# Performance work log

Measured on AMD Instinct MI355X. Metric: run time of the kernel, lower is better.

The kernel has to match this reference:

```python
import jax, jax.numpy as jnp
import numpy as np

N, C, H, W = 8, 256, 128, 128
HD = 256          # hidden_depth
FC, FS, CS = 8, 2, 8  # heads_count, fold_size, center_size
EPS_GN = 1e-5


def setup_inputs() -> dict:
    key = jax.random.key(0)
    ks = jax.random.split(key, 8)
    d = {
        'x': jax.random.normal(ks[0], (N, C, H, W), jnp.float32),
        'proj_w': jax.random.normal(ks[1], (2 * HD, C), jnp.float32) * 0.02,
        'proj_b': jnp.zeros((2 * HD,), jnp.float32),
        'merge_w': jax.random.normal(ks[2], (C, HD), jnp.float32) * 0.02,
        'merge_b': jnp.zeros((C,), jnp.float32),
        'alpha': jnp.ones((1,), jnp.float32),
        'beta': jnp.zeros((1,), jnp.float32),
        'g0_w': jnp.ones((C,), jnp.float32),
        'g0_b': jnp.zeros((C,), jnp.float32),
        'mlp_w0': jax.random.normal(ks[3], (2 * C, 2 * C), jnp.float32) * 0.02,
        'mlp_b0': jnp.zeros((2 * C,), jnp.float32),
        'mlp_w1': jax.random.normal(ks[4], (2 * C, C), jnp.float32) * 0.02,
        'mlp_b1': jnp.zeros((C,), jnp.float32),
        'g1_w': jnp.ones((C,), jnp.float32),
        'g1_b': jnp.zeros((C,), jnp.float32),
        'layer_scale': jnp.full((C,), 1e-5, jnp.float32),
    }
    return d


def _group_norm1(x, w, b):
    # GroupNorm(1, C): normalize over (C,H,W) per sample, per-channel affine
    mu = x.mean(axis=(1, 2, 3), keepdims=True)
    var = ((x - mu) ** 2).mean(axis=(1, 2, 3), keepdims=True)
    xn = (x - mu) * jax.lax.rsqrt(var + EPS_GN)
    return xn * w[None, :, None, None] + b[None, :, None, None]


def _l2norm(v):
    return v / jnp.maximum(jnp.linalg.norm(v, axis=-1, keepdims=True), 1e-12)


def _local_cluster(x, proj_w, proj_b, merge_w, merge_b, alpha, beta):
    n = x.shape[0]
    # 1x1 conv proj: C -> 2*HD
    y = jnp.einsum('nchw,oc->nohw', x, proj_w) + proj_b[None, :, None, None]
    c = y.shape[1] // FC              # per-head channels (2*HD/FC)
    h, w = H // FS, W // FS
    # 'n (fc c) (fh h) (fw w) -> (n fc fh fw) c h w'
    y = y.reshape(n, FC, c, FS, h, FS, w).transpose(0, 1, 3, 5, 2, 4, 6)
    y = y.reshape(n * FC * FS * FS, c, h, w)
    m = y.shape[0]
    # adaptive avg pool to CSxCS (h,w divisible by CS -> uniform pooling)
    center = y.reshape(m, c, CS, h // CS, CS, w // CS).mean(axis=(3, 5))
    L, s = h * w, CS * CS
    yf = y.reshape(m, c, L).transpose(0, 2, 1)       # [m, L, c]
    cf = center.reshape(m, c, s).transpose(0, 2, 1)  # [m, s, c]
    cv = c // 2
    x_point, x_value = yf[..., :cv], yf[..., cv:]
    c_point, c_value = cf[..., :cv], cf[..., cv:]
    sim = jnp.einsum('mlc,msc->mls', _l2norm(x_point), _l2norm(c_point))
    sim = jax.nn.sigmoid(alpha * sim + beta)         # [m, L, s]
    vals = sim.max(axis=2)                           # [m, L]
    idx = sim.argmax(axis=2) + s * jnp.arange(m)[:, None]
    vals = vals.reshape(-1)
    idx = idx.reshape(-1)
    xv = x_value.reshape(-1, cv)
    cvv = c_value.reshape(-1, cv)
    xv_aug = jnp.concatenate([xv, jnp.ones((xv.shape[0], 1), xv.dtype)], axis=1)
    cv_aug = jnp.concatenate([cvv, jnp.ones((cvv.shape[0], 1), cvv.dtype)], axis=1)
    # scatter-add weighted points into centers
    nc = cv_aug.at[idx].add(vals[:, None] * xv_aug)
    nc = nc[:, :-1] / nc[:, -1:]
    # gather back
    nx = vals[:, None] * nc[idx]                     # [m*L, cv]
    # '(n fc fh fw h w) c -> n (fc c) (fh h) (fw w)'
    nx = nx.reshape(n, FC, FS, FS, h, w, cv).transpose(0, 1, 6, 2, 4, 3, 5)
    nx = nx.reshape(n, FC * cv, H, W)                # [n, HD, H, W]
    return jnp.einsum('nchw,oc->nohw', nx, merge_w) + merge_b[None, :, None, None]


def reference(x, proj_w, proj_b, merge_w, merge_b, alpha, beta, g0_w, g0_b,
              mlp_w0, mlp_b0, mlp_w1, mlp_b1, g1_w, g1_b, layer_scale):
    new_x = _local_cluster(x, proj_w, proj_b, merge_w, merge_b, alpha, beta)
    new_x = _group_norm1(new_x, g0_w, g0_b)
    t = jnp.concatenate([x, new_x], axis=1)          # [n, 2C, H, W]
    t = t.transpose(0, 2, 3, 1)                      # NHWC
    t = jax.nn.gelu(t @ mlp_w0 + mlp_b0, approximate=False)
    t = t @ mlp_w1 + mlp_b1
    t = t.transpose(0, 3, 1, 2)                      # NCHW
    t = _group_norm1(t, g1_w, g1_b)
    t = t * layer_scale[None, :, None, None]
    return t + x
```

## Files before the change

### kernel.cpp

```cpp
#include <hip/hip_runtime.h>
#include <math.h>

#define PIX   16384
#define NB    8
#define CIN   256

typedef __attribute__((ext_vector_type(8))) short    short8;
typedef __attribute__((ext_vector_type(4))) float    f32x4;
typedef __attribute__((ext_vector_type(4))) unsigned short us4;
typedef __attribute__((ext_vector_type(8))) unsigned short us8;

__device__ __forceinline__ float bf2f(unsigned short h) {
  return __uint_as_float(((unsigned int)h) << 16);
}
__device__ __forceinline__ unsigned short f2bf(float f) {
  unsigned int u = __float_as_uint(f);
  return (unsigned short)((u + 0x7FFFu + ((u >> 16) & 1u)) >> 16);
}
__device__ __forceinline__ float gelu_f(float v) {
  return 0.5f * v * (1.f + erff(v * 0.70710678118654752f));
}

__device__ __forceinline__ float rowmax16(float v) {
  v = fmaxf(v, __uint_as_float(__builtin_amdgcn_update_dpp(
        __float_as_uint(v), __float_as_uint(v), 0x121, 0xF, 0xF, false)));
  v = fmaxf(v, __uint_as_float(__builtin_amdgcn_update_dpp(
        __float_as_uint(v), __float_as_uint(v), 0x122, 0xF, 0xF, false)));
  v = fmaxf(v, __uint_as_float(__builtin_amdgcn_update_dpp(
        __float_as_uint(v), __float_as_uint(v), 0x124, 0xF, 0xF, false)));
  v = fmaxf(v, __uint_as_float(__builtin_amdgcn_update_dpp(
        __float_as_uint(v), __float_as_uint(v), 0x128, 0xF, 0xF, false)));
  return v;
}

__global__ void zero_kernel(float* p, int n) {
  int i = blockIdx.x * blockDim.x + threadIdx.x;
  if (i < n) p[i] = 0.f;
}

__global__ void prep_weights(const float* __restrict__ pw_f, const float* __restrict__ mw_f,
                             const float* __restrict__ w0, const float* __restrict__ w1,
                             unsigned short* __restrict__ pw, unsigned short* __restrict__ mw,
                             unsigned short* __restrict__ w0t, unsigned short* __restrict__ w1t) {
  const int S1 = 512 * 256, S2 = 256 * 256, S3 = 512 * 512, S4 = 256 * 512;
  int i = blockIdx.x * 256 + threadIdx.x;
  if (i < S1) { pw[i] = f2bf(pw_f[i]); return; }
  i -= S1;
  if (i < S2) { mw[i] = f2bf(mw_f[i]); return; }
  i -= S2;
  if (i < S3) { int o = i >> 9, k = i & 511; w0t[i] = f2bf(w0[k * 512 + o]); return; }
  i -= S3;
  if (i < S4) { int o = i >> 9, k = i & 511; w1t[i] = f2bf(w1[k * 256 + o]); }
}

__global__ __launch_bounds__(256) void x_to_nhwc(const float* __restrict__ x,
                                                 unsigned short* __restrict__ xT) {
  __shared__ float tile[64][65];
  const int t = threadIdx.x;
  const int p0 = blockIdx.x * 64, c0 = blockIdx.y * 64, n = blockIdx.z;
#pragma unroll
  for (int i = 0; i < 4; i++) {
    const int c = i * 16 + (t >> 4);
    const float4 v = *(const float4*)(x + ((size_t)(n * 256 + c0 + c) << 14) + p0 + (t & 15) * 4);
    tile[c][(t & 15) * 4]     = v.x;
    tile[c][(t & 15) * 4 + 1] = v.y;
    tile[c][(t & 15) * 4 + 2] = v.z;
    tile[c][(t & 15) * 4 + 3] = v.w;
  }
  __syncthreads();
#pragma unroll
  for (int i = 0; i < 4; i++) {
    const int pp = i * 16 + (t >> 4);
    const int cl = (t & 15) * 4;
    us4 o;
    o.x = f2bf(tile[cl][pp]); o.y = f2bf(tile[cl + 1][pp]);
    o.z = f2bf(tile[cl + 2][pp]); o.w = f2bf(tile[cl + 3][pp]);
    *(us4*)&xT[(((size_t)n << 14) + p0 + pp) * 256 + c0 + cl] = o;
  }
}

template<bool CONCAT, bool GELU, bool STATS>
__global__ __launch_bounds__(256, 2) void mfma_gemm(
    const unsigned short* __restrict__ A, const float* __restrict__ bias,
    const unsigned short* __restrict__ B1, const unsigned short* __restrict__ B2,
    unsigned short* __restrict__ Y, int M, int K, int K1,
    int astride, int bstride, float* __restrict__ sums) {
  __shared__ unsigned short As[8192];
  __shared__ unsigned short Bs[8192];
  __shared__ float r1[4], r2[4];
  const int t = threadIdx.x;
  const int lane = t & 63, w = t >> 6;
  const int quad = lane >> 4, l16 = lane & 15;
  const int p0 = blockIdx.x * 128, m0 = blockIdx.y * 128;
  const int n = blockIdx.z;
  const int wm = w & 1, wn = w >> 1;
  const int K2 = K - K1;

  A += (size_t)n * astride;

  f32x4 acc[4][4];
#pragma unroll
  for (int im = 0; im < 4; im++)
#pragma unroll
    for (int in = 0; in < 4; in++) acc[im][in] = (f32x4)0.f;

  for (int k0 = 0; k0 < K; k0 += 64) {
    __syncthreads();
#pragma unroll
    for (int i = 0; i < 4; i++) {
      const int c = (w << 2) | i;
      const int tm = c >> 1, kk = c & 1;
      const int krow = k0 + kk * 32 + quad * 8;
      const unsigned short* ga = A + (size_t)(m0 + tm * 16 + l16) * K + krow;
      __builtin_amdgcn_global_load_lds((const __attribute__((address_space(1))) void*)ga,
          (__attribute__((address_space(3))) void*)&As[c * 512], 16, 0, 0);
      const int prow = p0 + tm * 16 + l16;
      const unsigned short* gb;
      if (!CONCAT || krow < K1)
        gb = B1 + ((((size_t)n << 14) + prow) * (size_t)K1) + krow;
      else
        gb = B2 + ((((size_t)n << 14) + prow) * (size_t)K2) + (krow - K1);
      __builtin_amdgcn_global_load_lds((const __attribute__((address_space(1))) void*)gb,
          (__attribute__((address_space(3))) void*)&Bs[c * 512], 16, 0, 0);
    }
    __syncthreads();
#pragma unroll
    for (int kk = 0; kk < 2; kk++) {
      short8 af[4], bfr[4];
#pragma unroll
      for (int im = 0; im < 4; im++)
        af[im] = *(const short8*)&As[(((wm * 4 + im) * 2 + kk) * 64 + lane) * 8];
#pragma unroll
      for (int in = 0; in < 4; in++)
        bfr[in] = *(const short8*)&Bs[(((wn * 4 + in) * 2 + kk) * 64 + lane) * 8];
#pragma unroll
      for (int im = 0; im < 4; im++)
#pragma unroll
        for (int in = 0; in < 4; in++)
          acc[im][in] = __builtin_amdgcn_mfma_f32_16x16x32_bf16(af[im], bfr[in], acc[im][in], 0, 0, 0);
    }
  }

  const size_t nb = ((size_t)n << 14);
  float s = 0.f, s2 = 0.f;
#pragma unroll
  for (int im = 0; im < 4; im++) {
    const int om = m0 + (wm * 4 + im) * 16 + quad * 4;
    const f32x4 bv = *(const f32x4*)(bias + (size_t)n * bstride + om);
#pragma unroll
    for (int in = 0; in < 4; in++) {
      const int p = p0 + (wn * 4 + in) * 16 + l16;
      float v0 = acc[im][in].x + bv.x;
      float v1 = acc[im][in].y + bv.y;
      float v2 = acc[im][in].z + bv.z;
      float v3 = acc[im][in].w + bv.w;
      if (GELU) { v0 = gelu_f(v0); v1 = gelu_f(v1); v2 = gelu_f(v2); v3 = gelu_f(v3); }
      if (STATS) {
        s += (v0 + v1) + (v2 + v3);
        s2 = fmaf(v0, v0, s2); s2 = fmaf(v1, v1, s2);
        s2 = fmaf(v2, v2, s2); s2 = fmaf(v3, v3, s2);
      }
      us4 o4;
      o4.x = f2bf(v0); o4.y = f2bf(v1); o4.z = f2bf(v2); o4.w = f2bf(v3);
      *(us4*)&Y[(nb + p) * M + om] = o4;
    }
  }
  if (STATS) {
#pragma unroll
    for (int off = 32; off > 0; off >>= 1) {
      s += __shfl_down(s, off);
      s2 += __shfl_down(s2, off);
    }
    if (lane == 0) { r1[w] = s; r2[w] = s2; }
    __syncthreads();
    if (t == 0) {
      atomicAdd(&sums[2 * n],     (r1[0] + r1[1]) + (r1[2] + r1[3]));
      atomicAdd(&sums[2 * n + 1], (r2[0] + r2[1]) + (r2[2] + r2[3]));
    }
  }
}


__global__ __launch_bounds__(256) void centers_kernel(
    const unsigned short* __restrict__ y, unsigned short* __restrict__ cpnh_g,
    float* __restrict__ cval_g) {
  const int m = blockIdx.y, slice = blockIdx.x;
  const int n = m >> 5, f = (m >> 2) & 7, s1 = (m >> 1) & 1, s2 = m & 1;
  const int t = threadIdx.x;
  __shared__ float cs[16][68];

  const size_t nbase = ((size_t)n << 14);
  const int prow0 = s1 * 64, pcol0 = s2 * 64, ch0 = f * 64;

  {
    const int bl = t >> 4;
    const int b = slice * 16 + bl;
    const int tid = t & 15, cg = tid & 7, ph = tid >> 3;
    const int pr0 = prow0 + (b >> 3) * 8 + ph * 4;
    const int pc0 = pcol0 + (b & 7) * 8;
    const unsigned short* yb = y + (nbase + (size_t)pr0 * 128 + pc0) * 512 + ch0 + cg * 8;
    float a8[8] = {0.f, 0.f, 0.f, 0.f, 0.f, 0.f, 0.f, 0.f};
#pragma unroll
    for (int r = 0; r < 4; r++) {
      us8 buf[8];
#pragma unroll
      for (int cc = 0; cc < 8; cc++)
        buf[cc] = *(const us8*)(yb + ((size_t)r * 128 + cc) * 512);
#pragma unroll
      for (int cc = 0; cc < 8; cc++)
#pragma unroll
        for (int j = 0; j < 8; j++) a8[j] += bf2f(buf[cc][j]);
    }
#pragma unroll
    for (int j = 0; j < 8; j++) a8[j] += __shfl_xor(a8[j], 8);
    if (ph == 0) {
      f32x4 o0, o1;
      o0.x = a8[0] * (1.f / 64.f); o0.y = a8[1] * (1.f / 64.f);
      o0.z = a8[2] * (1.f / 64.f); o0.w = a8[3] * (1.f / 64.f);
      o1.x = a8[4] * (1.f / 64.f); o1.y = a8[5] * (1.f / 64.f);
      o1.z = a8[6] * (1.f / 64.f); o1.w = a8[7] * (1.f / 64.f);
      *(f32x4*)&cs[bl][cg * 8]     = o0;
      *(f32x4*)&cs[bl][cg * 8 + 4] = o1;
    }
  }
  __syncthreads();

  if (t < 128) {
    const int bl = t >> 3, jg = t & 7;
    const int bg = slice * 16 + bl;
    if (jg < 8) {
      f32x4 ov;
      ov.x = cs[bl][32 + jg * 4]; ov.y = cs[bl][32 + jg * 4 + 1];
      ov.z = cs[bl][32 + jg * 4 + 2]; ov.w = cs[bl][32 + jg * 4 + 3];
      *(f32x4*)&cval_g[((size_t)(m * 64 + bg) << 5) + jg * 4] = ov;
    }
    float s = 0.f;
#pragma unroll
    for (int cc = 0; cc < 32; cc++) { const float v = cs[bl][cc]; s = fmaf(v, v, s); }
    const float inv = 1.f / fmaxf(sqrtf(s), 1e-12f);
    us4 o;
    o.x = f2bf(cs[bl][jg * 4] * inv);     o.y = f2bf(cs[bl][jg * 4 + 1] * inv);
    o.z = f2bf(cs[bl][jg * 4 + 2] * inv); o.w = f2bf(cs[bl][jg * 4 + 3] * inv);
    *(us4*)&cpnh_g[((size_t)(m * 64 + bg) << 5) + jg * 4] = o;
  }
}

__global__ __launch_bounds__(256, 8) void assign_kernel(
    const unsigned short* __restrict__ y, const unsigned short* __restrict__ cpnh_g,
    const float* __restrict__ alpha_p, const float* __restrict__ beta_p,
    float* __restrict__ svals_g, unsigned char* __restrict__ sbest_g,
    float* __restrict__ accp_v, float* __restrict__ accp_c) {
  const int m = blockIdx.y, slice = blockIdx.x;
  const int n = m >> 5, f = (m >> 2) & 7, s1 = (m >> 1) & 1, s2 = m & 1;
  const int t = threadIdx.x;
  const int wave = t >> 6, lane = t & 63;
  const int quad = lane >> 4, l16 = lane & 15;
  const float alpha = alpha_p[0], beta = beta_p[0];

  __shared__ float accv[64][34];

  for (int i = t; i < 64 * 34; i += 256) ((float*)accv)[i] = 0.f;

  const size_t nbase = ((size_t)n << 14);
  const int prow0 = s1 * 64, pcol0 = s2 * 64, ch0 = f * 64;

  const short8 cb0 = *(const short8*)&cpnh_g[((size_t)(m * 64 +  0 + l16) << 5) + quad * 8];
  const short8 cb1 = *(const short8*)&cpnh_g[((size_t)(m * 64 + 16 + l16) << 5) + quad * 8];
  const short8 cb2 = *(const short8*)&cpnh_g[((size_t)(m * 64 + 32 + l16) << 5) + quad * 8];
  const short8 cb3 = *(const short8*)&cpnh_g[((size_t)(m * 64 + 48 + l16) << 5) + quad * 8];
  const int sl4 = (((l16 >> 2) << 4) | (l16 & 3)) << 2;
  const int sh = quad << 4;
  __syncthreads();

  auto loadpt = [&](int tile, short8& a, short8& v) {
    const int pidx = slice * 512 + wave * 128 + tile * 16;
    const int pix = (prow0 + (pidx >> 6)) * 128 + pcol0 + (pidx & 63) + l16;
    const unsigned short* yp = y + (nbase + pix) * 512 + ch0 + quad * 8;
    a = *(const short8*)yp;
    v = *(const short8*)(yp + 32);
  };

  auto compute_tile = [&](int tile, short8 apt, short8 avl) {
    const int pidx = slice * 512 + wave * 128 + tile * 16;

    float nrm = 0.f;
#pragma unroll
    for (int j = 0; j < 8; j++) {
      const float fv = bf2f((unsigned short)apt[j]);
      nrm = fmaf(fv, fv, nrm);
    }
    nrm += __shfl_xor(nrm, 16);
    nrm += __shfl_xor(nrm, 32);
    const float inva = 1.f / fmaxf(sqrtf(nrm), 1e-12f);

    const f32x4 d0 = __builtin_amdgcn_mfma_f32_16x16x32_bf16(apt, cb0, (f32x4)0.f, 0, 0, 0);
    const f32x4 d1 = __builtin_amdgcn_mfma_f32_16x16x32_bf16(apt, cb1, (f32x4)0.f, 0, 0, 0);
    const f32x4 d2 = __builtin_amdgcn_mfma_f32_16x16x32_bf16(apt, cb2, (f32x4)0.f, 0, 0, 0);
    const f32x4 d3 = __builtin_amdgcn_mfma_f32_16x16x32_bf16(apt, cb3, (f32x4)0.f, 0, 0, 0);

    float bv[4]; int bi[4];
#pragma unroll
    for (int r = 0; r < 4; r++) {
      float v = fmaxf(fmaxf(d0[r], d1[r]), fmaxf(d2[r], d3[r]));
      v = rowmax16(v);
      bv[r] = v;
      const unsigned long long m0 = __ballot(d0[r] == v);
      const unsigned long long m1 = __ballot(d1[r] == v);
      const unsigned long long m2 = __ballot(d2[r] == v);
      const unsigned long long m3 = __ballot(d3[r] == v);
      const unsigned f0 = (unsigned)(m0 >> sh) & 0xFFFFu;
      const unsigned f1 = (unsigned)(m1 >> sh) & 0xFFFFu;
      const unsigned f2 = (unsigned)(m2 >> sh) & 0xFFFFu;
      const unsigned f3 = (unsigned)(m3 >> sh) & 0xFFFFu;
      int ii = 48 + __ffs(f3) - 1;
      if (f2) ii = 32 + __ffs(f2) - 1;
      if (f1) ii = 16 + __ffs(f1) - 1;
      if (f0) ii = __ffs(f0) - 1;
      bi[r] = ii;
    }

    const float rv01 = (l16 & 1) ? bv[1] : bv[0];
    const float rv23 = (l16 & 1) ? bv[3] : bv[2];
    const float rowv = (l16 & 2) ? rv23 : rv01;
    const int   ri01 = (l16 & 1) ? bi[1] : bi[0];
    const int   ri23 = (l16 & 1) ? bi[3] : bi[2];
    const int   rowi = (l16 & 2) ? ri23 : ri01;
    const unsigned pk = (__float_as_uint(rowv) & ~63u) | (unsigned)rowi;
    const unsigned got = (unsigned)__builtin_amdgcn_ds_bpermute(sl4, (int)pk);
    const int   idx = (int)(got & 63u);
    const float dot = __uint_as_float(got & ~63u);

    const float val = 1.f / (1.f + __expf(-fmaf(alpha, dot * inva, beta)));
    if (quad == 0) {
      svals_g[(size_t)m * 4096 + pidx + l16] = val;
      sbest_g[(size_t)m * 4096 + pidx + l16] = (unsigned char)idx;
    }
#pragma unroll
    for (int j = 0; j < 8; j++)
      atomicAdd(&accv[idx][quad * 8 + j], val * bf2f((unsigned short)avl[j]));
    if (quad == 0) atomicAdd(&accv[idx][32], val);
  };

  {
    short8 a0, v0, a1 = {}, v1 = {};
    loadpt(0, a0, v0);
#pragma unroll 1
    for (int tp = 0; tp < 8; tp++) {
      if (tp < 7) loadpt(tp + 1, a1, v1);
      compute_tile(tp, a0, v0);
      a0 = a1; v0 = v1;
    }
  }
  __syncthreads();

  const size_t pb = ((size_t)(m * 8 + slice)) * 64;
  for (int i = t; i < 2048; i += 256) {
    const int b = i >> 5, q = i & 31;
    accp_v[(pb + b) * 32 + q] = accv[b][q];
  }
  if (t < 64) accp_c[pb + t] = accv[t][32];
}

__global__ __launch_bounds__(256) void gather_kernel(
    const float* __restrict__ accp_v, const float* __restrict__ accp_c,
    const float* __restrict__ cval_g, const float* __restrict__ svals_g,
    const unsigned char* __restrict__ sbest_g, unsigned short* __restrict__ nx) {
  const int m = blockIdx.y, slice = blockIdx.x;
  const int n = m >> 5, f = (m >> 2) & 7, s1 = (m >> 1) & 1, s2 = m & 1;
  const int t = threadIdx.x;
  __shared__ float cm[64][34];

  const size_t nbase = ((size_t)n << 14);
  const int prow0 = s1 * 64, pcol0 = s2 * 64;

  for (int i = t; i < 2048; i += 256) {
    const int b = i >> 5, q = i & 31;
    float s = cval_g[((size_t)(m * 64 + b) << 5) + q];
    float c = 1.f;
#pragma unroll
    for (int s8 = 0; s8 < 8; s8++) {
      const size_t pb = ((size_t)(m * 8 + s8)) * 64 + b;
      s += accp_v[pb * 32 + q];
      c += accp_c[pb];
    }
    cm[b][q] = s / c;
  }
  __syncthreads();

#pragma unroll
  for (int pass = 0; pass < 2; pass++) {
    const int l = slice * 512 + pass * 256 + t;
    const int p = (prow0 + (l >> 6)) * 128 + pcol0 + (l & 63);
    const float v = svals_g[(size_t)m * 4096 + l];
    const int b = sbest_g[(size_t)m * 4096 + l];
    unsigned short* nr = nx + (nbase + p) * 256 + f * 32;
#pragma unroll
    for (int q8 = 0; q8 < 4; q8++) {
      const float2 a0 = *(const float2*)&cm[b][q8 * 8];
      const float2 a1 = *(const float2*)&cm[b][q8 * 8 + 2];
      const float2 a2 = *(const float2*)&cm[b][q8 * 8 + 4];
      const float2 a3 = *(const float2*)&cm[b][q8 * 8 + 6];
      us8 o;
      o[0] = f2bf(v * a0.x); o[1] = f2bf(v * a0.y);
      o[2] = f2bf(v * a1.x); o[3] = f2bf(v * a1.y);
      o[4] = f2bf(v * a2.x); o[5] = f2bf(v * a2.y);
      o[6] = f2bf(v * a3.x); o[7] = f2bf(v * a3.y);
      *(us8*)&nr[q8 * 8] = o;
    }
  }
}

__global__ void gn_finalize0(const float* __restrict__ sums, const float* __restrict__ g0w,
                             const float* __restrict__ g0b, float* __restrict__ scl,
                             float* __restrict__ bia) {
  const int n = blockIdx.x, c = threadIdx.x;
  const float cntinv = 1.f / (float)(CIN * PIX);
  const float mu = sums[2 * n] * cntinv;
  const float var = sums[2 * n + 1] * cntinv - mu * mu;
  const float rs = rsqrtf(var + 1e-5f);
  const float a = rs * g0w[c];
  scl[n * 256 + c] = a;
  bia[n * 256 + c] = g0b[c] - mu * a;
}

__global__ void w0_scale(const unsigned short* __restrict__ w0t,
                         const float* __restrict__ scl, unsigned short* __restrict__ w0s) {
  const int n = blockIdx.y;
  const int i = blockIdx.x * 256 + threadIdx.x;
  const int k = i & 511;
  unsigned short v = w0t[i];
  if (k >= 256) v = f2bf(bf2f(v) * scl[n * 256 + k - 256]);
  w0s[(size_t)n * 262144 + i] = v;
}

__global__ void b0_eff(const unsigned short* __restrict__ w0t, const float* __restrict__ b0,
                       const float* __restrict__ bia, float* __restrict__ b0e) {
  const int n = blockIdx.y;
  const int o = blockIdx.x * 256 + threadIdx.x;
  float s = b0[o];
  const unsigned short* wr = w0t + (size_t)o * 512 + 256;
  const float* br = bia + n * 256;
#pragma unroll 4
  for (int k = 0; k < 256; k++) s = fmaf(bf2f(wr[k]), br[k], s);
  b0e[n * 512 + o] = s;
}

__global__ __launch_bounds__(256) void final_transpose(
    const unsigned short* __restrict__ u, const float* __restrict__ x,
    const float* __restrict__ sums, const float* __restrict__ g1w,
    const float* __restrict__ g1b, const float* __restrict__ lsc,
    float* __restrict__ out) {
  __shared__ float tile[64][68];
  const int t = threadIdx.x;
  const int p0 = blockIdx.x * 64, c0 = blockIdx.y * 64, n = blockIdx.z;
  {
    const int pl = t >> 2, g = t & 3;
    const unsigned short* up = u + ((((size_t)n << 14) + p0 + pl) << 8) + c0 + g * 16;
    const us8 v0 = *(const us8*)up;
    const us8 v1 = *(const us8*)(up + 8);
#pragma unroll
    for (int j = 0; j < 8; j++) {
      tile[pl][g * 16 + j] = bf2f(v0[j]);
      tile[pl][g * 16 + 8 + j] = bf2f(v1[j]);
    }
  }
  __syncthreads();
  {
    const int cl = t >> 2, g = t & 3;
    const int c = c0 + cl;
    const float cntinv = 1.f / (float)(CIN * PIX);
    const float mu = sums[2 * n] * cntinv;
    const float var = sums[2 * n + 1] * cntinv - mu * mu;
    const float rs = rsqrtf(var + 1e-5f);
    const float gw = rs * g1w[c] * lsc[c];
    const float gb = (g1b[c] - mu * rs * g1w[c]) * lsc[c];
    const size_t rowb = ((size_t)(n * 256 + c) << 14) + p0 + g * 16;
#pragma unroll
    for (int q = 0; q < 4; q++) {
      const float4 xv = *(const float4*)(x + rowb + q * 4);
      float4 o;
      o.x = fmaf(tile[g * 16 + q * 4][cl], gw, gb) + xv.x;
      o.y = fmaf(tile[g * 16 + q * 4 + 1][cl], gw, gb) + xv.y;
      o.z = fmaf(tile[g * 16 + q * 4 + 2][cl], gw, gb) + xv.z;
      o.w = fmaf(tile[g * 16 + q * 4 + 3][cl], gw, gb) + xv.w;
      *(float4*)(out + rowb + q * 4) = o;
    }
  }
}

extern "C" void kernel_launch(void* const* d_in, const int* in_sizes, int n_in,
                              void* d_out, int out_size, void* d_ws, size_t ws_size,
                              hipStream_t stream) {
  const float* x       = (const float*)d_in[0];
  const float* proj_w  = (const float*)d_in[1];
  const float* proj_b  = (const float*)d_in[2];
  const float* merge_w = (const float*)d_in[3];
  const float* merge_b = (const float*)d_in[4];
  const float* alpha   = (const float*)d_in[5];
  const float* beta    = (const float*)d_in[6];
  const float* g0w     = (const float*)d_in[7];
  const float* g0b     = (const float*)d_in[8];
  const float* w0      = (const float*)d_in[9];
  const float* b0      = (const float*)d_in[10];
  const float* w1      = (const float*)d_in[11];
  const float* b1      = (const float*)d_in[12];
  const float* g1w     = (const float*)d_in[13];
  const float* g1b     = (const float*)d_in[14];
  const float* lsc     = (const float*)d_in[15];
  float* out = (float*)d_out;

  unsigned short* wsu = (unsigned short*)d_ws;
  unsigned short* xT  = wsu;
  unsigned short* y   = xT + (size_t)33554432;
  unsigned short* nx  = y + (size_t)67108864;
  unsigned short* pw  = nx + (size_t)33554432;
  unsigned short* mw  = pw + 131072;
  unsigned short* w0t = mw + 65536;
  unsigned short* w1t = w0t + 262144;
  unsigned short* w0s = w1t + 131072;
  float* sums = (float*)(w0s + (size_t)2097152);
  float* scl0 = sums + 32;
  float* bia0 = scl0 + 2048;
  float* b0e  = bia0 + 2048;
  unsigned short* newx = (unsigned short*)d_out;

  float* svals_g = (float*)((char*)d_out + 67108864);
  float* cval_g  = svals_g + 1048576;
  float* accp_v  = cval_g + 524288;
  float* accp_c  = accp_v + 4194304;
  unsigned short* cpnh_g = (unsigned short*)(accp_c + 131072);
  unsigned char*  sbest_g = (unsigned char*)(cpnh_g + 524288);

  zero_kernel<<<1, 64, 0, stream>>>(sums, 32);
  prep_weights<<<2304, 256, 0, stream>>>(proj_w, merge_w, w0, w1, pw, mw, w0t, w1t);
  x_to_nhwc<<<dim3(256, 4, NB), 256, 0, stream>>>(x, xT);

  mfma_gemm<false, false, false><<<dim3(128, 4, NB), 256, 0, stream>>>(
      pw, proj_b, xT, nullptr, y, 512, 256, 256, 0, 0, nullptr);

  centers_kernel<<<dim3(4, 256), 256, 0, stream>>>(y, cpnh_g, cval_g);
  assign_kernel<<<dim3(8, 256), 256, 0, stream>>>(
      y, cpnh_g, alpha, beta, svals_g, sbest_g, accp_v, accp_c);
  gather_kernel<<<dim3(8, 256), 256, 0, stream>>>(
      accp_v, accp_c, cval_g, svals_g, sbest_g, nx);

  mfma_gemm<false, false, true><<<dim3(128, 2, NB), 256, 0, stream>>>(
      mw, merge_b, nx, nullptr, newx, 256, 256, 256, 0, 0, sums);

  gn_finalize0<<<NB, 256, 0, stream>>>(sums, g0w, g0b, scl0, bia0);
  w0_scale<<<dim3(1024, NB), 256, 0, stream>>>(w0t, scl0, w0s);
  b0_eff<<<dim3(2, NB), 256, 0, stream>>>(w0t, b0, bia0, b0e);

  mfma_gemm<true, true, false><<<dim3(128, 4, NB), 256, 0, stream>>>(
      w0s, b0e, xT, newx, y, 512, 512, 256, 262144, 512, nullptr);

  mfma_gemm<false, false, true><<<dim3(128, 2, NB), 256, 0, stream>>>(
      w1t, b1, y, nullptr, nx, 256, 512, 512, 0, 0, sums + 16);

  final_transpose<<<dim3(256, 4, NB), 256, 0, stream>>>(
      nx, x, sums + 16, g1w, g1b, lsc, out);
}
```

Measured before the change: 1.007 ms.

## Load GEMM fragments directly from global memory; hoist assign loads; compile-time K

The MFMA GEMM no longer stages A and B tiles through LDS with global_load_lds and barriers. Each wave now reads its bf16 fragments straight from global memory into registers, and K is a template constant so the loop fully unrolls. The assign kernel issues all eight tile loads up front before computing, and its occupancy hint drops from 8 to 4 blocks per SM to allow more registers. The aim is to remove LDS round-trips and barrier stalls, at the cost of redundant global or cache traffic and higher register pressure.

```diff
diff --git a/kernel.cpp b/kernel.cpp
--- a/kernel.cpp
+++ b/kernel.cpp
@@ -79,14 +79,12 @@
   }
 }
 
-template<bool CONCAT, bool GELU, bool STATS>
-__global__ __launch_bounds__(256, 2) void mfma_gemm(
+template<int KI, int K1I, bool CONCAT, bool GELU, bool STATS>
+__global__ __launch_bounds__(256, 2) void mfma_gemm_v2(
     const unsigned short* __restrict__ A, const float* __restrict__ bias,
     const unsigned short* __restrict__ B1, const unsigned short* __restrict__ B2,
-    unsigned short* __restrict__ Y, int M, int K, int K1,
+    unsigned short* __restrict__ Y, int M,
     int astride, int bstride, float* __restrict__ sums) {
-  __shared__ unsigned short As[8192];
-  __shared__ unsigned short Bs[8192];
   __shared__ float r1[4], r2[4];
   const int t = threadIdx.x;
   const int lane = t & 63, w = t >> 6;
@@ -94,9 +92,15 @@
   const int p0 = blockIdx.x * 128, m0 = blockIdx.y * 128;
   const int n = blockIdx.z;
   const int wm = w & 1, wn = w >> 1;
-  const int K2 = K - K1;
+  constexpr int K2I = (KI - K1I) > 0 ? (KI - K1I) : 1;
 
   A += (size_t)n * astride;
+  const size_t nb = ((size_t)n << 14);
+
+  const unsigned short* abase  = A + (size_t)(m0 + wm * 64 + l16) * KI + quad * 8;
+  const unsigned short* b1base = B1 + (nb + p0 + wn * 64 + l16) * (size_t)K1I + quad * 8;
+  const unsigned short* b2base = CONCAT
+      ? B2 + (nb + p0 + wn * 64 + l16) * (size_t)K2I + quad * 8 : B1;
 
   f32x4 acc[4][4];
 #pragma unroll
@@ -104,44 +108,26 @@
 #pragma unroll
     for (int in = 0; in < 4; in++) acc[im][in] = (f32x4)0.f;
 
-  for (int k0 = 0; k0 < K; k0 += 64) {
-    __syncthreads();
-#pragma unroll
-    for (int i = 0; i < 4; i++) {
-      const int c = (w << 2) | i;
-      const int tm = c >> 1, kk = c & 1;
-      const int krow = k0 + kk * 32 + quad * 8;
-      const unsigned short* ga = A + (size_t)(m0 + tm * 16 + l16) * K + krow;
-      __builtin_amdgcn_global_load_lds((const __attribute__((address_space(1))) void*)ga,
-          (__attribute__((address_space(3))) void*)&As[c * 512], 16, 0, 0);
-      const int prow = p0 + tm * 16 + l16;
-      const unsigned short* gb;
-      if (!CONCAT || krow < K1)
-        gb = B1 + ((((size_t)n << 14) + prow) * (size_t)K1) + krow;
+#pragma unroll
+  for (int ks = 0; ks < KI / 32; ks++) {
+    short8 af[4], bfr[4];
+#pragma unroll
+    for (int im = 0; im < 4; im++)
+      af[im] = *(const short8*)(abase + (size_t)im * 16 * KI + ks * 32);
+#pragma unroll
+    for (int in = 0; in < 4; in++) {
+      if (!CONCAT || (ks * 32) < K1I)
+        bfr[in] = *(const short8*)(b1base + (size_t)in * 16 * K1I + ks * 32);
       else
-        gb = B2 + ((((size_t)n << 14) + prow) * (size_t)K2) + (krow - K1);
-      __builtin_amdgcn_global_load_lds((const __attribute__((address_space(1))) void*)gb,
-          (__attribute__((address_space(3))) void*)&Bs[c * 512], 16, 0, 0);
-    }
-    __syncthreads();
-#pragma unroll
-    for (int kk = 0; kk < 2; kk++) {
-      short8 af[4], bfr[4];
-#pragma unroll
-      for (int im = 0; im < 4; im++)
-        af[im] = *(const short8*)&As[(((wm * 4 + im) * 2 + kk) * 64 + lane) * 8];
+        bfr[in] = *(const short8*)(b2base + (size_t)in * 16 * K2I + (ks * 32 - K1I));
+    }
+#pragma unroll
+    for (int im = 0; im < 4; im++)
 #pragma unroll
       for (int in = 0; in < 4; in++)
-        bfr[in] = *(const short8*)&Bs[(((wn * 4 + in) * 2 + kk) * 64 + lane) * 8];
-#pragma unroll
-      for (int im = 0; im < 4; im++)
-#pragma unroll
-        for (int in = 0; in < 4; in++)
-          acc[im][in] = __builtin_amdgcn_mfma_f32_16x16x32_bf16(af[im], bfr[in], acc[im][in], 0, 0, 0);
-    }
-  }
-
-  const size_t nb = ((size_t)n << 14);
+        acc[im][in] = __builtin_amdgcn_mfma_f32_16x16x32_bf16(af[im], bfr[in], acc[im][in], 0, 0, 0);
+  }
+
   float s = 0.f, s2 = 0.f;
 #pragma unroll
   for (int im = 0; im < 4; im++) {
@@ -245,7 +231,7 @@
   }
 }
 
-__global__ __launch_bounds__(256, 8) void assign_kernel(
+__global__ __launch_bounds__(256, 4) void assign_kernel(
     const unsigned short* __restrict__ y, const unsigned short* __restrict__ cpnh_g,
     const float* __restrict__ alpha_p, const float* __restrict__ beta_p,
     float* __restrict__ svals_g, unsigned char* __restrict__ sbest_g,
@@ -342,14 +328,13 @@
   };
 
   {
-    short8 a0, v0, a1 = {}, v1 = {};
-    loadpt(0, a0, v0);
-#pragma unroll 1
-    for (int tp = 0; tp < 8; tp++) {
-      if (tp < 7) loadpt(tp + 1, a1, v1);
-      compute_tile(tp, a0, v0);
-      a0 = a1; v0 = v1;
-    }
+    short8 a0, v0, a1, v1, a2, v2, a3, v3, a4, v4, a5, v5, a6, v6, a7, v7;
+    loadpt(0, a0, v0); loadpt(1, a1, v1); loadpt(2, a2, v2); loadpt(3, a3, v3);
+    loadpt(4, a4, v4); loadpt(5, a5, v5); loadpt(6, a6, v6); loadpt(7, a7, v7);
+    compute_tile(0, a0, v0); compute_tile(1, a1, v1);
+    compute_tile(2, a2, v2); compute_tile(3, a3, v3);
+    compute_tile(4, a4, v4); compute_tile(5, a5, v5);
+    compute_tile(6, a6, v6); compute_tile(7, a7, v7);
   }
   __syncthreads();
 
@@ -535,8 +520,8 @@
   prep_weights<<<2304, 256, 0, stream>>>(proj_w, merge_w, w0, w1, pw, mw, w0t, w1t);
   x_to_nhwc<<<dim3(256, 4, NB), 256, 0, stream>>>(x, xT);
 
-  mfma_gemm<false, false, false><<<dim3(128, 4, NB), 256, 0, stream>>>(
-      pw, proj_b, xT, nullptr, y, 512, 256, 256, 0, 0, nullptr);
+  mfma_gemm_v2<256, 256, false, false, false><<<dim3(128, 4, NB), 256, 0, stream>>>(
+      pw, proj_b, xT, nullptr, y, 512, 0, 0, nullptr);
 
   centers_kernel<<<dim3(4, 256), 256, 0, stream>>>(y, cpnh_g, cval_g);
   assign_kernel<<<dim3(8, 256), 256, 0, stream>>>(
@@ -544,18 +529,18 @@
   gather_kernel<<<dim3(8, 256), 256, 0, stream>>>(
       accp_v, accp_c, cval_g, svals_g, sbest_g, nx);
 
-  mfma_gemm<false, false, true><<<dim3(128, 2, NB), 256, 0, stream>>>(
-      mw, merge_b, nx, nullptr, newx, 256, 256, 256, 0, 0, sums);
+  mfma_gemm_v2<256, 256, false, false, true><<<dim3(128, 2, NB), 256, 0, stream>>>(
+      mw, merge_b, nx, nullptr, newx, 256, 0, 0, sums);
 
   gn_finalize0<<<NB, 256, 0, stream>>>(sums, g0w, g0b, scl0, bia0);
   w0_scale<<<dim3(1024, NB), 256, 0, stream>>>(w0t, scl0, w0s);
   b0_eff<<<dim3(2, NB), 256, 0, stream>>>(w0t, b0, bia0, b0e);
 
-  mfma_gemm<true, true, false><<<dim3(128, 4, NB), 256, 0, stream>>>(
-      w0s, b0e, xT, newx, y, 512, 512, 256, 262144, 512, nullptr);
-
-  mfma_gemm<false, false, true><<<dim3(128, 2, NB), 256, 0, stream>>>(
-      w1t, b1, y, nullptr, nx, 256, 512, 512, 0, 0, sums + 16);
+  mfma_gemm_v2<512, 256, true, true, false><<<dim3(128, 4, NB), 256, 0, stream>>>(
+      w0s, b0e, xT, newx, y, 512, 262144, 512, nullptr);
+
+  mfma_gemm_v2<512, 512, false, false, true><<<dim3(128, 2, NB), 256, 0, stream>>>(
+      w1t, b1, y, nullptr, nx, 256, 0, 0, sums + 16);
 
   final_transpose<<<dim3(256, 4, NB), 256, 0, stream>>>(
       nx, x, sums + 16, g1w, g1b, lsc, out);
```

Measured after the change: 1.197 ms. +18.9%, slower.

## Replace ballot argmax with DPP integer reductions, preload all tiles, retune launch bounds

Applied to the files above, without the earlier changes.

The per-row argmax in assign_kernel now maps floats to monotone unsigned keys, reduces the max with DPP, and finds the first matching index with a DPP integer min, replacing four ballots plus ffs logic. All eight point tiles are loaded up front instead of software-pipelined one tile ahead, which exposes more memory parallelism at the cost of registers. To allow for that, assign_kernel's launch bounds drop from 8 to 4 waves per SIMD, while mfma_gemm's rise from 2 to 4, which may force register spilling in the GEMM.

```diff
diff --git a/kernel.cpp b/kernel.cpp
--- a/kernel.cpp
+++ b/kernel.cpp
@@ -21,15 +21,25 @@
   return 0.5f * v * (1.f + erff(v * 0.70710678118654752f));
 }
 
-__device__ __forceinline__ float rowmax16(float v) {
-  v = fmaxf(v, __uint_as_float(__builtin_amdgcn_update_dpp(
-        __float_as_uint(v), __float_as_uint(v), 0x121, 0xF, 0xF, false)));
-  v = fmaxf(v, __uint_as_float(__builtin_amdgcn_update_dpp(
-        __float_as_uint(v), __float_as_uint(v), 0x122, 0xF, 0xF, false)));
-  v = fmaxf(v, __uint_as_float(__builtin_amdgcn_update_dpp(
-        __float_as_uint(v), __float_as_uint(v), 0x124, 0xF, 0xF, false)));
-  v = fmaxf(v, __uint_as_float(__builtin_amdgcn_update_dpp(
-        __float_as_uint(v), __float_as_uint(v), 0x128, 0xF, 0xF, false)));
+__device__ __forceinline__ unsigned fmono(float f) {
+  const unsigned u = __float_as_uint(f);
+  return (u & 0x80000000u) ? ~u : (u | 0x80000000u);
+}
+
+__device__ __forceinline__ unsigned umax16(unsigned v) {
+  unsigned t;
+  t = (unsigned)__builtin_amdgcn_update_dpp((int)v, (int)v, 0x121, 0xF, 0xF, false); v = v > t ? v : t;
+  t = (unsigned)__builtin_amdgcn_update_dpp((int)v, (int)v, 0x122, 0xF, 0xF, false); v = v > t ? v : t;
+  t = (unsigned)__builtin_amdgcn_update_dpp((int)v, (int)v, 0x124, 0xF, 0xF, false); v = v > t ? v : t;
+  t = (unsigned)__builtin_amdgcn_update_dpp((int)v, (int)v, 0x128, 0xF, 0xF, false); v = v > t ? v : t;
+  return v;
+}
+__device__ __forceinline__ int imin16(int v) {
+  int t;
+  t = __builtin_amdgcn_update_dpp(v, v, 0x121, 0xF, 0xF, false); v = v < t ? v : t;
+  t = __builtin_amdgcn_update_dpp(v, v, 0x122, 0xF, 0xF, false); v = v < t ? v : t;
+  t = __builtin_amdgcn_update_dpp(v, v, 0x124, 0xF, 0xF, false); v = v < t ? v : t;
+  t = __builtin_amdgcn_update_dpp(v, v, 0x128, 0xF, 0xF, false); v = v < t ? v : t;
   return v;
 }
 
@@ -80,7 +90,7 @@
 }
 
 template<bool CONCAT, bool GELU, bool STATS>
-__global__ __launch_bounds__(256, 2) void mfma_gemm(
+__global__ __launch_bounds__(256, 4) void mfma_gemm(
     const unsigned short* __restrict__ A, const float* __restrict__ bias,
     const unsigned short* __restrict__ B1, const unsigned short* __restrict__ B2,
     unsigned short* __restrict__ Y, int M, int K, int K1,
@@ -245,7 +255,7 @@
   }
 }
 
-__global__ __launch_bounds__(256, 8) void assign_kernel(
+__global__ __launch_bounds__(256, 4) void assign_kernel(
     const unsigned short* __restrict__ y, const unsigned short* __restrict__ cpnh_g,
     const float* __restrict__ alpha_p, const float* __restrict__ beta_p,
     float* __restrict__ svals_g, unsigned char* __restrict__ sbest_g,
@@ -269,7 +279,6 @@
   const short8 cb2 = *(const short8*)&cpnh_g[((size_t)(m * 64 + 32 + l16) << 5) + quad * 8];
   const short8 cb3 = *(const short8*)&cpnh_g[((size_t)(m * 64 + 48 + l16) << 5) + quad * 8];
   const int sl4 = (((l16 >> 2) << 4) | (l16 & 3)) << 2;
-  const int sh = quad << 4;
   __syncthreads();
 
   auto loadpt = [&](int tile, short8& a, short8& v) {
@@ -301,22 +310,24 @@
     float bv[4]; int bi[4];
 #pragma unroll
     for (int r = 0; r < 4; r++) {
-      float v = fmaxf(fmaxf(d0[r], d1[r]), fmaxf(d2[r], d3[r]));
-      v = rowmax16(v);
-      bv[r] = v;
-      const unsigned long long m0 = __ballot(d0[r] == v);
-      const unsigned long long m1 = __ballot(d1[r] == v);
-      const unsigned long long m2 = __ballot(d2[r] == v);
-      const unsigned long long m3 = __ballot(d3[r] == v);
-      const unsigned f0 = (unsigned)(m0 >> sh) & 0xFFFFu;
-      const unsigned f1 = (unsigned)(m1 >> sh) & 0xFFFFu;
-      const unsigned f2 = (unsigned)(m2 >> sh) & 0xFFFFu;
-      const unsigned f3 = (unsigned)(m3 >> sh) & 0xFFFFu;
-      int ii = 48 + __ffs(f3) - 1;
-      if (f2) ii = 32 + __ffs(f2) - 1;
-      if (f1) ii = 16 + __ffs(f1) - 1;
-      if (f0) ii = __ffs(f0) - 1;
-      bi[r] = ii;
+      const unsigned u0 = fmono(d0[r]);
+      const unsigned u1 = fmono(d1[r]);
+      const unsigned u2 = fmono(d2[r]);
+      const unsigned u3 = fmono(d3[r]);
+      unsigned mx = u0 > u1 ? u0 : u1;
+      const unsigned mxb = u2 > u3 ? u2 : u3;
+      mx = mx > mxb ? mx : mxb;
+      mx = umax16(mx);
+      int c0 = (u0 == mx) ? l16        : 64;
+      int c1 = (u1 == mx) ? (16 + l16) : 64;
+      int c2 = (u2 == mx) ? (32 + l16) : 64;
+      int c3 = (u3 == mx) ? (48 + l16) : 64;
+      int ci = c0 < c1 ? c0 : c1;
+      const int cb = c2 < c3 ? c2 : c3;
+      ci = ci < cb ? ci : cb;
+      ci = imin16(ci);
+      bi[r] = ci;
+      bv[r] = __uint_as_float((mx & 0x80000000u) ? (mx ^ 0x80000000u) : ~mx);
     }
 
     const float rv01 = (l16 & 1) ? bv[1] : bv[0];
@@ -342,14 +353,13 @@
   };
 
   {
-    short8 a0, v0, a1 = {}, v1 = {};
-    loadpt(0, a0, v0);
-#pragma unroll 1
-    for (int tp = 0; tp < 8; tp++) {
-      if (tp < 7) loadpt(tp + 1, a1, v1);
-      compute_tile(tp, a0, v0);
-      a0 = a1; v0 = v1;
-    }
+    short8 a0, v0, a1, v1, a2, v2, a3, v3, a4, v4, a5, v5, a6, v6, a7, v7;
+    loadpt(0, a0, v0); loadpt(1, a1, v1); loadpt(2, a2, v2); loadpt(3, a3, v3);
+    loadpt(4, a4, v4); loadpt(5, a5, v5); loadpt(6, a6, v6); loadpt(7, a7, v7);
+    compute_tile(0, a0, v0); compute_tile(1, a1, v1);
+    compute_tile(2, a2, v2); compute_tile(3, a3, v3);
+    compute_tile(4, a4, v4); compute_tile(5, a5, v5);
+    compute_tile(6, a6, v6); compute_tile(7, a7, v7);
   }
   __syncthreads();
 
```

Measured after the change: 1.003 ms. Within noise of the previous version (-0.4%).
